# Kernel optimization log

Measured on AMD Instinct MI355X. Metric: run time of the kernel, lower is better.

Reference implementation:

```python
import jax, jax.numpy as jnp
import numpy as np

H, W, C = 96, 96, 21
SIGMA_RGB = 3.0   # bilateral spatial sdims (as called in the original code)
SIGMA_XY = 64.0   # gaussian spatial sdims
SCHAN = 255.0     # bilateral color std
COMPAT = 10.0     # Potts compatibility weight (same for both kernels)
N_ITERS = 5


def _gauss_kernel(feats):
    # feats: [N, D] -> K[i,j] = exp(-0.5 * ||f_i - f_j||^2)
    sq = jnp.sum(feats * feats, axis=-1)
    d2 = sq[:, None] + sq[None, :] - 2.0 * (feats @ feats.T)
    return jnp.exp(-0.5 * jnp.maximum(d2, 0.0))


def setup_inputs() -> dict:
    key = jax.random.key(0)
    k1, k2, k3 = jax.random.split(key, 3)
    logits = jax.random.normal(k1, (1, C, H, W), dtype=jnp.float32)
    labels = jax.random.randint(k2, (1, H, W), 0, C, dtype=jnp.int32)
    image = jax.random.uniform(k3, (1, 3, H, W), dtype=jnp.float32) * 255.0
    return {"logits": logits, "labels": labels, "image": image, "num_classes": C}


def reference(logits, labels, image, num_classes):
    # unary potentials: U = -log_softmax(logits)
    logp = jax.nn.log_softmax(logits, axis=1)              # [1,C,H,W]
    U = (-logp)[0].reshape(num_classes, -1).T              # [N,C]

    # pixel features
    yy, xx = jnp.meshgrid(jnp.arange(H), jnp.arange(W), indexing="ij")
    pos = jnp.stack([yy, xx], axis=-1).reshape(-1, 2).astype(logits.dtype)  # [N,2]
    rgb = image[0].transpose(1, 2, 0).reshape(-1, 3)        # [N,3]

    # dense pairwise kernels (exact Gaussian / bilateral, self-connection removed)
    N = H * W
    eye = jnp.eye(N, dtype=logits.dtype)
    Kg = _gauss_kernel(pos / SIGMA_XY) - eye
    fb = jnp.concatenate([pos / SIGMA_RGB, rgb / SCHAN], axis=-1)
    Kb = _gauss_kernel(fb) - eye

    # mean-field inference, Potts compatibility mu(l,l') = [l != l']
    Q0 = jax.nn.softmax(-U, axis=1)                         # [N,C]

    def step(Q, _):
        msg = Kg @ Q + Kb @ Q                               # [N,C] filtered Q
        pair = COMPAT * (jnp.sum(msg, axis=1, keepdims=True) - msg)
        Q = jax.nn.softmax(-U - pair, axis=1)
        return Q, None

    Q, _ = jax.lax.scan(step, Q0, None, length=N_ITERS)
    pairwise = Q.T.reshape(1, num_classes, H, W)

    # cross entropy (mean over pixels)
    ce = -jnp.mean(jnp.take_along_axis(logp, labels[:, None].astype(jnp.int32), axis=1))

    return ce + pairwise                                    # broadcast, as in original
```

## Files before the change

### kernel.cpp

```cpp
#include <hip/hip_runtime.h>
#include <hip/hip_fp16.h>

#define HH 96
#define WW 96
#define CC 21
#define NN (HH*WW)
#define NBLK (NN/256)
#define STRIDE 24
#define ROWF (WW*STRIDE)
#define NRUN (NN/8)

typedef _Float16 f16x8 __attribute__((ext_vector_type(8)));
typedef float f32x4 __attribute__((ext_vector_type(4)));

union H8 { f16x8 v; __half2 h2[4]; };


__global__ __launch_bounds__(256) void k_setup(
    const float* __restrict__ logits, const int* __restrict__ labels,
    const float* __restrict__ image, float* __restrict__ U,
    float* __restrict__ Q0, _Float16* __restrict__ QTa,
    _Float16* __restrict__ QTb, float* __restrict__ gtab,
    float* __restrict__ partial) {
  const int t = threadIdx.x;
  const int i = blockIdx.x * 256 + t;
  const int qoff = (i >> 3) * 192 + (i & 7);

  float d[CC];
  float mx = -1e30f;
#pragma unroll
  for (int c = 0; c < CC; ++c) {
    d[c] = logits[c * NN + i];
    mx = fmaxf(mx, d[c]);
  }
  float s = 0.f;
#pragma unroll
  for (int c = 0; c < CC; ++c) { d[c] -= mx; s += __expf(d[c]); }
  const float lse = logf(s);
  const float inv = 1.f / s;
  const int lab = labels[i];
  float myU = 0.f;
#pragma unroll
  for (int c = 0; c < CC; ++c) {
    const float Uc = lse - d[c];
    const float q = __expf(d[c]) * inv;
    U[i * STRIDE + c] = Uc;
    Q0[i * STRIDE + c] = q;
    QTa[qoff + c * 8] = (_Float16)q;
    myU = (c == lab) ? Uc : myU;
  }
  const float rr = image[i] * (1.f / 255.f);
  const float rg = image[NN + i] * (1.f / 255.f);
  const float rb = image[2 * NN + i] * (1.f / 255.f);
  U[i * STRIDE + 21] = 0.f;
  U[i * STRIDE + 22] = 0.f;
  U[i * STRIDE + 23] = 0.f;
  Q0[i * STRIDE + 21] = rr;
  Q0[i * STRIDE + 22] = rg;
  Q0[i * STRIDE + 23] = rb;
  QTa[qoff + 21 * 8] = (_Float16)rr;
  QTa[qoff + 22 * 8] = (_Float16)rg;
  QTa[qoff + 23 * 8] = (_Float16)rb;
  QTb[qoff + 21 * 8] = (_Float16)rr;
  QTb[qoff + 22 * 8] = (_Float16)rg;
  QTb[qoff + 23 * 8] = (_Float16)rb;

  if (blockIdx.x == 0 && t < 96) {
    const float dv = (float)t * (1.f / 64.f);
    gtab[t] = __expf(-0.5f * dv * dv);
  }

  __shared__ float red[256];
  red[t] = myU;
  __syncthreads();
  for (int off = 128; off > 0; off >>= 1) {
    if (t < off) red[t] += red[t + off];
    __syncthreads();
  }
  if (t == 0) partial[blockIdx.x] = red[0];
}

__global__ __launch_bounds__(256) void k_gauss_y(
    const float* __restrict__ Qin, float* __restrict__ Gy,
    const float* __restrict__ gtab) {
  __shared__ float g[96];
  if (threadIdx.x < 96) g[threadIdx.x] = gtab[threadIdx.x];
  __syncthreads();
  const int idx = blockIdx.x * 256 + threadIdx.x;
  const int y = idx / ROWF;
  const int rem = idx - y * ROWF;
  const float* base = Qin + rem;
  float a0 = 0.f, a1 = 0.f, a2 = 0.f, a3 = 0.f;
#pragma unroll 6
  for (int yp = 0; yp < HH; yp += 4) {
    a0 = fmaf(g[abs(y - yp)], base[yp * ROWF], a0);
    a1 = fmaf(g[abs(y - yp - 1)], base[(yp + 1) * ROWF], a1);
    a2 = fmaf(g[abs(y - yp - 2)], base[(yp + 2) * ROWF], a2);
    a3 = fmaf(g[abs(y - yp - 3)], base[(yp + 3) * ROWF], a3);
  }
  Gy[idx] = (a0 + a1) + (a2 + a3);
}

__global__ __launch_bounds__(512) void k_bilat(
    const float* __restrict__ U, const float* __restrict__ Qin,
    const float* __restrict__ Gy, const _Float16* __restrict__ QT,
    const float* __restrict__ gtab, float* __restrict__ Qout,
    _Float16* __restrict__ QTout, const float* __restrict__ partial,
    float* __restrict__ out, int last) {
  __shared__ __half sytab[64];
  __shared__ __half2 sxtab[64];
  __shared__ float sgt[96];
  __shared__ float psum[8][16][24];
  __shared__ float sces;

  const int tid = threadIdx.x;
  const int w = tid >> 6;
  const int l = tid & 63;
  const int g = l >> 4;
  const int q = l & 15;

  if (tid < 64) {
    const float dv = (float)(tid - 32);
    sytab[tid] = __float2half(__expf(dv * dv * (-1.f / 18.f)));
    const float dv1 = dv + 1.f;
    sxtab[tid] = __floats2half2_rn(__expf(dv * dv * (-1.f / 18.f)),
                                   __expf(dv1 * dv1 * (-1.f / 18.f)));
    if (last) {
      float v = (tid < NBLK) ? partial[tid] : 0.f;
#pragma unroll
      for (int off = 32; off >= 1; off >>= 1) v += __shfl_xor(v, off, 64);
      if (tid == 0) sces = v * (1.f / (float)NN);
    }
  } else if (tid < 160) {
    sgt[tid - 64] = gtab[tid - 64];
  }
  __syncthreads();

  const int tile = blockIdx.x;
  const int ty0 = (tile / 24) * 4;
  const int tx0 = (tile - (tile / 24) * 24) * 4;

  const int pr = q >> 2, pc = q & 3;
  const int yi = ty0 + pr, xi = tx0 + pc;
  const int ipix = yi * WW + xi;

  const float4 rown = *(const float4*)(Qin + ipix * STRIDE + 20);
  const __half2 ri_r = __float2half2_rn(rown.y);
  const __half2 ri_g = __float2half2_rn(rown.z);
  const __half2 ri_b = __float2half2_rn(rown.w);
  const __half2 mhalf = __floats2half2_rn(-0.5f, -0.5f);
  const __half hzero = __float2half(0.f);

  const int xs = tx0 - 16;
  const int xbase0 = (xs > 0 ? xs : 0) & ~7;
  const int rid0 = (w < 4) ? w * 23 : 92 + (w - 4) * 22;
  const int nrun = (w < 4) ? 23 : 22;

  const int row2 = (16 + q > 23) ? 23 : 16 + q;

  f32x4 acc0 = {0.f, 0.f, 0.f, 0.f};
  f32x4 acc1 = {0.f, 0.f, 0.f, 0.f};

#pragma unroll
  for (int ck = 0; ck < 6; ++ck) {
    const int r = ck * 4 + g;
    const int rid = rid0 + r;
    const int wr = rid / 5;
    const int cs = rid - wr * 5;
    const int yj = ty0 - 16 + wr;
    const int xb = xbase0 + cs * 8;
    const bool ok = (r < nrun) & (yj >= 0) & (yj < HH) & (xb <= WW - 8);
    const int yc = min(max(yj, 0), HH - 1);
    const int xc = min(xb, WW - 8);
    const _Float16* base = QT + (yc * 12 + (xc >> 3)) * 192;

    H8 b1, b2, rj, gj, bj;
    b1.v = *(const f16x8*)(base + q * 8);
    b2.v = *(const f16x8*)(base + row2 * 8);
    rj.v = *(const f16x8*)(base + 21 * 8);
    gj.v = *(const f16x8*)(base + 22 * 8);
    bj.v = *(const f16x8*)(base + 23 * 8);

    const int dy = yj - yi;
    const int iy = min(max(dy + 32, 0), 63);
    const __half syv = ok ? sytab[iy] : hzero;
    const __half2 sy2 = __half2half2(syv);
    const int dx0 = xb - xi;
    const int ix0 = min(max(dx0 + 32, 0), 57);

    H8 af;
#pragma unroll
    for (int e2 = 0; e2 < 4; ++e2) {
      const __half2 sx2 = sxtab[ix0 + 2 * e2];
      const __half2 dr = __hsub2(rj.h2[e2], ri_r);
      const __half2 dg = __hsub2(gj.h2[e2], ri_g);
      const __half2 db = __hsub2(bj.h2[e2], ri_b);
      __half2 d2c = __hmul2(dr, dr);
      d2c = __hfma2(dg, dg, d2c);
      d2c = __hfma2(db, db, d2c);
      const __half2 ec = h2exp(__hmul2(d2c, mhalf));
      af.h2[e2] = __hmul2(__hmul2(sy2, sx2), ec);
    }
    acc0 = __builtin_amdgcn_mfma_f32_16x16x32_f16(af.v, b1.v, acc0, 0, 0, 0);
    acc1 = __builtin_amdgcn_mfma_f32_16x16x32_f16(af.v, b2.v, acc1, 0, 0, 0);
  }

#pragma unroll
  for (int reg = 0; reg < 4; ++reg) {
    psum[w][g * 4 + reg][q] = acc0[reg];
    if (q < 8) psum[w][g * 4 + reg][16 + q] = acc1[reg];
  }
  __syncthreads();

  const int half_ = l >> 5;
  const int cl = l & 31;
  const bool act = cl < CC;
  const int pix = w * 2 + half_;
  const int py = ty0 + (pix >> 2), px = tx0 + (pix & 3);
  const int ip = py * WW + px;
  float Qic = 0.f;
  if (cl < STRIDE) Qic = Qin[ip * STRIDE + cl];
  float tcv = 0.f, Uc = 0.f, Gc = 0.f;
  if (act) {
    tcv = psum[0][pix][cl] + psum[1][pix][cl] + psum[2][pix][cl] +
          psum[3][pix][cl] + psum[4][pix][cl] + psum[5][pix][cl] +
          psum[6][pix][cl] + psum[7][pix][cl];
    Uc = U[ip * STRIDE + cl];
    const float* grow = Gy + py * ROWF + cl;
    float g0 = 0.f, g1 = 0.f, g2 = 0.f, g3 = 0.f;
#pragma unroll 6
    for (int xp = 0; xp < WW; xp += 4) {
      g0 = fmaf(sgt[abs(px - xp)], grow[xp * STRIDE], g0);
      g1 = fmaf(sgt[abs(px - xp - 1)], grow[(xp + 1) * STRIDE], g1);
      g2 = fmaf(sgt[abs(px - xp - 2)], grow[(xp + 2) * STRIDE], g2);
      g3 = fmaf(sgt[abs(px - xp - 3)], grow[(xp + 3) * STRIDE], g3);
    }
    Gc = (g0 + g1) + (g2 + g3);
  }
  const float contrib = act ? (tcv + Gc - 2.f * Qic) : 0.f;
  float tot = contrib;
#pragma unroll
  for (int off = 16; off >= 1; off >>= 1) tot += __shfl_xor(tot, off, 32);
  const float lc = act ? (-Uc - 10.f * (tot - contrib)) : -1e30f;
  float mxl = lc;
#pragma unroll
  for (int off = 16; off >= 1; off >>= 1)
    mxl = fmaxf(mxl, __shfl_xor(mxl, off, 32));
  const float e = act ? __expf(lc - mxl) : 0.f;
  float se = e;
#pragma unroll
  for (int off = 16; off >= 1; off >>= 1) se += __shfl_xor(se, off, 32);
  const float qnew = e / se;
  if (last) {
    if (act) out[cl * NN + ip] = sces + qnew;
  } else {
    if (cl < STRIDE) Qout[ip * STRIDE + cl] = act ? qnew : Qic;
    if (act) QTout[(ip >> 3) * 192 + cl * 8 + (ip & 7)] = (_Float16)qnew;
  }
}

extern "C" void kernel_launch(void* const* d_in, const int* in_sizes, int n_in,
                              void* d_out, int out_size, void* d_ws,
                              size_t ws_size, hipStream_t stream) {
  const float* logits = (const float*)d_in[0];
  const int* labels = (const int*)d_in[1];
  const float* image = (const float*)d_in[2];
  float* ws = (float*)d_ws;

  float* U = ws;
  float* Qa = U + NN * STRIDE;
  float* Qb = Qa + NN * STRIDE;
  float* Gy = Qb + NN * STRIDE;
  float* gtab = Gy + NN * STRIDE;
  float* partial = gtab + 96;
  float* cepad = partial + 64;
  _Float16* QTa = (_Float16*)(cepad + 64);
  _Float16* QTb = QTa + NRUN * 192;

  k_setup<<<NBLK, 256, 0, stream>>>(logits, labels, image, U, Qa, QTa, QTb,
                                    gtab, partial);

  const float* qi = Qa;
  float* qo = Qb;
  const _Float16* qti = QTa;
  _Float16* qto = QTb;
  const int gblk = NN * STRIDE / 256;
  for (int it = 0; it < 5; ++it) {
    k_gauss_y<<<gblk, 256, 0, stream>>>(qi, Gy, gtab);
    k_bilat<<<576, 512, 0, stream>>>(U, qi, Gy, qti, gtab, qo, qto, partial,
                                     (float*)d_out, it == 4);
    qi = qo;
    qo = (qo == Qb) ? Qa : Qb;
    const _Float16* tmp = qti;
    qti = qto;
    qto = (_Float16*)tmp;
  }
}
```

Baseline: 138.2 us.

## Stage bilateral window of QT into shared memory in two halves

The bilateral kernel now cooperatively copies the 36-row neighbourhood window of the fp16 QT tiles into LDS in two 18-row halves. The MFMA loop then reads its B operands and rgb features from shared memory instead of global memory. Launch bounds also request 4 blocks of 512 threads per CU. This adds about 37KB of LDS per block and extra barriers, which may limit occupancy and adds a staging copy of data each wave previously read only once.

New measurement: 146.3 us. 5.8% more time.

```diff
diff --git a/kernel.cpp b/kernel.cpp
--- a/kernel.cpp
+++ b/kernel.cpp
@@ -101,16 +101,17 @@
   Gy[idx] = (a0 + a1) + (a2 + a3);
 }
 
-__global__ __launch_bounds__(512) void k_bilat(
+__global__ __launch_bounds__(512, 4) void k_bilat(
     const float* __restrict__ U, const float* __restrict__ Qin,
     const float* __restrict__ Gy, const _Float16* __restrict__ QT,
     const float* __restrict__ gtab, float* __restrict__ Qout,
     _Float16* __restrict__ QTout, const float* __restrict__ partial,
     float* __restrict__ out, int last) {
+  __shared__ _Float16 swin[90 * 208];
+  __shared__ float psum[8][16][24];
   __shared__ __half sytab[64];
   __shared__ __half2 sxtab[64];
   __shared__ float sgt[96];
-  __shared__ float psum[8][16][24];
   __shared__ float sces;
 
   const int tid = threadIdx.x;
@@ -134,7 +135,6 @@
   } else if (tid < 160) {
     sgt[tid - 64] = gtab[tid - 64];
   }
-  __syncthreads();
 
   const int tile = blockIdx.x;
   const int ty0 = (tile / 24) * 4;
@@ -153,8 +153,8 @@
 
   const int xs = tx0 - 16;
   const int xbase0 = (xs > 0 ? xs : 0) & ~7;
-  const int rid0 = (w < 4) ? w * 23 : 92 + (w - 4) * 22;
-  const int nrun = (w < 4) ? 23 : 22;
+  const int rid0h = (w < 2) ? 12 * w : 24 + 11 * (w - 2);
+  const int nrunh = (w < 2) ? 12 : 11;
 
   const int row2 = (16 + q > 23) ? 23 : 16 + q;
 
@@ -162,47 +162,67 @@
   f32x4 acc1 = {0.f, 0.f, 0.f, 0.f};
 
 #pragma unroll
-  for (int ck = 0; ck < 6; ++ck) {
-    const int r = ck * 4 + g;
-    const int rid = rid0 + r;
-    const int wr = rid / 5;
-    const int cs = rid - wr * 5;
-    const int yj = ty0 - 16 + wr;
-    const int xb = xbase0 + cs * 8;
-    const bool ok = (r < nrun) & (yj >= 0) & (yj < HH) & (xb <= WW - 8);
-    const int yc = min(max(yj, 0), HH - 1);
-    const int xc = min(xb, WW - 8);
-    const _Float16* base = QT + (yc * 12 + (xc >> 3)) * 192;
-
-    H8 b1, b2, rj, gj, bj;
-    b1.v = *(const f16x8*)(base + q * 8);
-    b2.v = *(const f16x8*)(base + row2 * 8);
-    rj.v = *(const f16x8*)(base + 21 * 8);
-    gj.v = *(const f16x8*)(base + 22 * 8);
-    bj.v = *(const f16x8*)(base + 23 * 8);
-
-    const int dy = yj - yi;
-    const int iy = min(max(dy + 32, 0), 63);
-    const __half syv = ok ? sytab[iy] : hzero;
-    const __half2 sy2 = __half2half2(syv);
-    const int dx0 = xb - xi;
-    const int ix0 = min(max(dx0 + 32, 0), 57);
-
-    H8 af;
-#pragma unroll
-    for (int e2 = 0; e2 < 4; ++e2) {
-      const __half2 sx2 = sxtab[ix0 + 2 * e2];
-      const __half2 dr = __hsub2(rj.h2[e2], ri_r);
-      const __half2 dg = __hsub2(gj.h2[e2], ri_g);
-      const __half2 db = __hsub2(bj.h2[e2], ri_b);
-      __half2 d2c = __hmul2(dr, dr);
-      d2c = __hfma2(dg, dg, d2c);
-      d2c = __hfma2(db, db, d2c);
-      const __half2 ec = h2exp(__hmul2(d2c, mhalf));
-      af.h2[e2] = __hmul2(__hmul2(sy2, sx2), ec);
+  for (int h = 0; h < 2; ++h) {
+    const int h18 = h * 18;
+    __syncthreads();
+#pragma unroll
+    for (int k = 0; k < 5; ++k) {
+      const int c = tid + (k << 9);
+      if (c < 2160) {
+        const int rb = c / 24;
+        const int part = c - rb * 24;
+        const int rr = rb / 5, cs = rb - rr * 5;
+        const int yj = ty0 - 16 + h18 + rr;
+        const int yc = min(max(yj, 0), HH - 1);
+        const int xc = min(xbase0 + cs * 8, WW - 8);
+        const f16x8 v =
+            *(const f16x8*)(QT + (yc * 12 + (xc >> 3)) * 192 + part * 8);
+        *(f16x8*)(swin + rb * 208 + part * 8) = v;
+      }
     }
-    acc0 = __builtin_amdgcn_mfma_f32_16x16x32_f16(af.v, b1.v, acc0, 0, 0, 0);
-    acc1 = __builtin_amdgcn_mfma_f32_16x16x32_f16(af.v, b2.v, acc1, 0, 0, 0);
+    __syncthreads();
+
+#pragma unroll
+    for (int ck = 0; ck < 3; ++ck) {
+      const int r = ck * 4 + g;
+      const int rh = min(rid0h + r, 89);
+      const int rr = rh / 5, cs = rh - rr * 5;
+      const int yj = ty0 - 16 + h18 + rr;
+      const int xb = xbase0 + cs * 8;
+      const bool ok = (r < nrunh) & (yj >= 0) & (yj < HH) & (xb <= WW - 8);
+      const _Float16* base = swin + rh * 208;
+
+      H8 b1, b2, rj, gj, bj;
+      b1.v = *(const f16x8*)(base + q * 8);
+      b2.v = *(const f16x8*)(base + row2 * 8);
+      rj.v = *(const f16x8*)(base + 21 * 8);
+      gj.v = *(const f16x8*)(base + 22 * 8);
+      bj.v = *(const f16x8*)(base + 23 * 8);
+
+      const int dy = yj - yi;
+      const int iy = min(max(dy + 32, 0), 63);
+      const __half syv = ok ? sytab[iy] : hzero;
+      const __half2 sy2 = __half2half2(syv);
+      const int dx0 = xb - xi;
+      const int ix0 = min(max(dx0 + 32, 0), 57);
+
+      H8 af;
+#pragma unroll
+      for (int e2 = 0; e2 < 4; ++e2) {
+        const __half2 sx2 = sxtab[ix0 + 2 * e2];
+        const __half2 dr = __hsub2(rj.h2[e2], ri_r);
+        const __half2 dg = __hsub2(gj.h2[e2], ri_g);
+        const __half2 db = __hsub2(bj.h2[e2], ri_b);
+        __half2 d2c = __hmul2(dr, dr);
+        d2c = __hfma2(dg, dg, d2c);
+        d2c = __hfma2(db, db, d2c);
+        const __half2 ec = h2exp(__hmul2(d2c, mhalf));
+        af.h2[e2] = __hmul2(__hmul2(sy2, sx2), ec);
+      }
+      acc0 = __builtin_amdgcn_mfma_f32_16x16x32_f16(af.v, b1.v, acc0, 0, 0, 0);
+      acc1 = __builtin_amdgcn_mfma_f32_16x16x32_f16(af.v, b2.v, acc1, 0, 0, 0);
+    }
+    __syncthreads();
   }
 
 #pragma unroll
```

## Fuse vertical Gaussian pass into bilateral kernel via shared-memory recompute

Applied to the files above, without the earlier changes.

Removes the separate k_gauss_y launch and its global Gy buffer. Each bilateral tile block now computes the y-direction Gaussian for its own 4 image rows across the full width into shared memory, then runs the x pass from LDS. The Gaussian tables are now built inside the block rather than read from a global table. This trades one launch per iteration and a global round-trip for redundant work: every one of the 576 blocks reads the whole Q field and does a full column sum. It also adds about 36 KB of shared memory per block, which may lower occupancy.

Result: slower. 319.8 us (+131.4%).

```diff
diff --git a/kernel.cpp b/kernel.cpp
--- a/kernel.cpp
+++ b/kernel.cpp
@@ -9,6 +9,7 @@
 #define STRIDE 24
 #define ROWF (WW*STRIDE)
 #define NRUN (NN/8)
+#define NTILE 576
 
 typedef _Float16 f16x8 __attribute__((ext_vector_type(8)));
 typedef float f32x4 __attribute__((ext_vector_type(4)));
@@ -20,8 +21,7 @@
     const float* __restrict__ logits, const int* __restrict__ labels,
     const float* __restrict__ image, float* __restrict__ U,
     float* __restrict__ Q0, _Float16* __restrict__ QTa,
-    _Float16* __restrict__ QTb, float* __restrict__ gtab,
-    float* __restrict__ partial) {
+    _Float16* __restrict__ QTb, float* __restrict__ partial) {
   const int t = threadIdx.x;
   const int i = blockIdx.x * 256 + t;
   const int qoff = (i >> 3) * 192 + (i & 7);
@@ -65,11 +65,6 @@
   QTb[qoff + 22 * 8] = (_Float16)rg;
   QTb[qoff + 23 * 8] = (_Float16)rb;
 
-  if (blockIdx.x == 0 && t < 96) {
-    const float dv = (float)t * (1.f / 64.f);
-    gtab[t] = __expf(-0.5f * dv * dv);
-  }
-
   __shared__ float red[256];
   red[t] = myU;
   __syncthreads();
@@ -80,37 +75,16 @@
   if (t == 0) partial[blockIdx.x] = red[0];
 }
 
-__global__ __launch_bounds__(256) void k_gauss_y(
-    const float* __restrict__ Qin, float* __restrict__ Gy,
-    const float* __restrict__ gtab) {
-  __shared__ float g[96];
-  if (threadIdx.x < 96) g[threadIdx.x] = gtab[threadIdx.x];
-  __syncthreads();
-  const int idx = blockIdx.x * 256 + threadIdx.x;
-  const int y = idx / ROWF;
-  const int rem = idx - y * ROWF;
-  const float* base = Qin + rem;
-  float a0 = 0.f, a1 = 0.f, a2 = 0.f, a3 = 0.f;
-#pragma unroll 6
-  for (int yp = 0; yp < HH; yp += 4) {
-    a0 = fmaf(g[abs(y - yp)], base[yp * ROWF], a0);
-    a1 = fmaf(g[abs(y - yp - 1)], base[(yp + 1) * ROWF], a1);
-    a2 = fmaf(g[abs(y - yp - 2)], base[(yp + 2) * ROWF], a2);
-    a3 = fmaf(g[abs(y - yp - 3)], base[(yp + 3) * ROWF], a3);
-  }
-  Gy[idx] = (a0 + a1) + (a2 + a3);
-}
-
 __global__ __launch_bounds__(512) void k_bilat(
     const float* __restrict__ U, const float* __restrict__ Qin,
-    const float* __restrict__ Gy, const _Float16* __restrict__ QT,
-    const float* __restrict__ gtab, float* __restrict__ Qout,
+    const _Float16* __restrict__ QT, float* __restrict__ Qout,
     _Float16* __restrict__ QTout, const float* __restrict__ partial,
     float* __restrict__ out, int last) {
+  __shared__ float sGy[4 * ROWF];
+  __shared__ float psum[8][16][24];
   __shared__ __half sytab[64];
   __shared__ __half2 sxtab[64];
   __shared__ float sgt[96];
-  __shared__ float psum[8][16][24];
   __shared__ float sces;
 
   const int tid = threadIdx.x;
@@ -119,26 +93,51 @@
   const int g = l >> 4;
   const int q = l & 15;
 
-  if (tid < 64) {
-    const float dv = (float)(tid - 32);
-    sytab[tid] = __float2half(__expf(dv * dv * (-1.f / 18.f)));
-    const float dv1 = dv + 1.f;
-    sxtab[tid] = __floats2half2_rn(__expf(dv * dv * (-1.f / 18.f)),
-                                   __expf(dv1 * dv1 * (-1.f / 18.f)));
-    if (last) {
-      float v = (tid < NBLK) ? partial[tid] : 0.f;
-#pragma unroll
-      for (int off = 32; off >= 1; off >>= 1) v += __shfl_xor(v, off, 64);
-      if (tid == 0) sces = v * (1.f / (float)NN);
-    }
-  } else if (tid < 160) {
-    sgt[tid - 64] = gtab[tid - 64];
-  }
-  __syncthreads();
-
   const int tile = blockIdx.x;
   const int ty0 = (tile / 24) * 4;
   const int tx0 = (tile - (tile / 24) * 24) * 4;
+
+  if (tid < 96) {
+    const float dv = (float)tid * (1.f / 64.f);
+    sgt[tid] = __expf(-0.5f * dv * dv);
+  }
+  if (tid >= 128 && tid < 192) {
+    const int k = tid - 128;
+    const float dv = (float)(k - 32);
+    sytab[k] = __float2half(__expf(dv * dv * (-1.f / 18.f)));
+    const float dv1 = dv + 1.f;
+    sxtab[k] = __floats2half2_rn(__expf(dv * dv * (-1.f / 18.f)),
+                                 __expf(dv1 * dv1 * (-1.f / 18.f)));
+  }
+  if (last && tid < 64) {
+    float v = (tid < NBLK) ? partial[tid] : 0.f;
+#pragma unroll
+    for (int off = 32; off >= 1; off >>= 1) v += __shfl_xor(v, off, 64);
+    if (tid == 0) sces = v * (1.f / (float)NN);
+  }
+  __syncthreads();
+
+#pragma unroll
+  for (int k = 0; k < 5; ++k) {
+    const int p = tid + (k << 9);
+    if (p < ROWF) {
+      const float* col = Qin + p;
+      float a0 = 0.f, a1 = 0.f, a2 = 0.f, a3 = 0.f;
+#pragma unroll 6
+      for (int yp = 0; yp < HH; ++yp) {
+        const float v = col[yp * ROWF];
+        const int d = ty0 - yp;
+        a0 = fmaf(sgt[abs(d)], v, a0);
+        a1 = fmaf(sgt[abs(d + 1)], v, a1);
+        a2 = fmaf(sgt[abs(d + 2)], v, a2);
+        a3 = fmaf(sgt[abs(d + 3)], v, a3);
+      }
+      sGy[0 * ROWF + p] = a0;
+      sGy[1 * ROWF + p] = a1;
+      sGy[2 * ROWF + p] = a2;
+      sGy[3 * ROWF + p] = a3;
+    }
+  }
 
   const int pr = q >> 2, pc = q & 3;
   const int yi = ty0 + pr, xi = tx0 + pc;
@@ -155,7 +154,6 @@
   const int xbase0 = (xs > 0 ? xs : 0) & ~7;
   const int rid0 = (w < 4) ? w * 23 : 92 + (w - 4) * 22;
   const int nrun = (w < 4) ? 23 : 22;
-
   const int row2 = (16 + q > 23) ? 23 : 16 + q;
 
   f32x4 acc0 = {0.f, 0.f, 0.f, 0.f};
@@ -226,7 +224,7 @@
           psum[3][pix][cl] + psum[4][pix][cl] + psum[5][pix][cl] +
           psum[6][pix][cl] + psum[7][pix][cl];
     Uc = U[ip * STRIDE + cl];
-    const float* grow = Gy + py * ROWF + cl;
+    const float* grow = sGy + (pix >> 2) * ROWF + cl;
     float g0 = 0.f, g1 = 0.f, g2 = 0.f, g3 = 0.f;
 #pragma unroll 6
     for (int xp = 0; xp < WW; xp += 4) {
@@ -270,25 +268,21 @@
   float* U = ws;
   float* Qa = U + NN * STRIDE;
   float* Qb = Qa + NN * STRIDE;
-  float* Gy = Qb + NN * STRIDE;
-  float* gtab = Gy + NN * STRIDE;
-  float* partial = gtab + 96;
+  float* partial = Qb + NN * STRIDE;
   float* cepad = partial + 64;
   _Float16* QTa = (_Float16*)(cepad + 64);
   _Float16* QTb = QTa + NRUN * 192;
 
   k_setup<<<NBLK, 256, 0, stream>>>(logits, labels, image, U, Qa, QTa, QTb,
-                                    gtab, partial);
+                                    partial);
 
   const float* qi = Qa;
   float* qo = Qb;
   const _Float16* qti = QTa;
   _Float16* qto = QTb;
-  const int gblk = NN * STRIDE / 256;
   for (int it = 0; it < 5; ++it) {
-    k_gauss_y<<<gblk, 256, 0, stream>>>(qi, Gy, gtab);
-    k_bilat<<<576, 512, 0, stream>>>(U, qi, Gy, qti, gtab, qo, qto, partial,
-                                     (float*)d_out, it == 4);
+    k_bilat<<<NTILE, 512, 0, stream>>>(U, qi, qti, qo, qto, partial,
+                                       (float*)d_out, it == 4);
     qi = qo;
     qo = (qo == Qb) ? Qa : Qb;
     const _Float16* tmp = qti;
```
